# Optimization experiments

Hardware: AMD Instinct MI355X
Metric: run time of the kernel (lower is better)

Reference implementation:

```python
import jax, jax.numpy as jnp
import numpy as np

N = 100000          # active voxels
KS = 7              # kernel size per spatial dim
K = KS ** 3         # 343 kernel offsets
G = 64              # voxel grid extent
INPLANES = 128
PLANES = 128
D2 = PLANES // 4    # 32
EPS = 1e-5


def _build_neighbor_map(seed=0):
    # Random distinct voxel coordinates in a G^3 grid, then for every point and
    # every 7^3 offset find the index of the neighboring voxel (-1 if absent).
    rng = np.random.default_rng(seed)
    lin = rng.choice(G ** 3, size=N, replace=False)
    coords = np.stack(np.unravel_index(lin, (G, G, G)), axis=1).astype(np.int64)  # [N,3]
    keys = coords[:, 0] * G * G + coords[:, 1] * G + coords[:, 2]
    order = np.argsort(keys)
    skeys = keys[order]
    offs = np.arange(KS) - KS // 2
    off_grid = np.stack(np.meshgrid(offs, offs, offs, indexing='ij'), axis=-1).reshape(K, 3)
    q = coords[:, None, :] + off_grid[None, :, :]          # [N,K,3]
    inb = np.all((q >= 0) & (q < G), axis=-1)
    qk = q[..., 0] * G * G + q[..., 1] * G + q[..., 2]
    pos = np.searchsorted(skeys, qk)
    pos_c = np.clip(pos, 0, N - 1)
    found = inb & (skeys[pos_c] == qk)
    nbr = np.where(found, order[pos_c], -1).astype(np.int32)  # [N,K]
    return jnp.asarray(nbr)


def setup_inputs() -> dict:
    key = jax.random.key(0)
    k = jax.random.split(key, 4)
    feats = jax.random.normal(k[0], (N, INPLANES), jnp.float32)
    w1 = jax.random.normal(k[1], (INPLANES, D2), jnp.float32) / np.sqrt(INPLANES)
    w_conv = jax.random.normal(k[2], (K, D2, D2), jnp.float32) / np.sqrt(K * D2)
    w2 = jax.random.normal(k[3], (D2, PLANES), jnp.float32) / np.sqrt(D2)
    return {
        'feats': feats,
        'nbr': _build_neighbor_map(),
        'w1': w1,
        'ln1_g': jnp.ones((D2,), jnp.float32),
        'ln1_b': jnp.zeros((D2,), jnp.float32),
        'w_conv': w_conv,
        'w2': w2,
        'ln2_g': jnp.ones((PLANES,), jnp.float32),
        'ln2_b': jnp.zeros((PLANES,), jnp.float32),
    }


def _layernorm(x, g, b):
    m = jnp.mean(x, axis=-1, keepdims=True)
    v = jnp.var(x, axis=-1, keepdims=True)
    return (x - m) * jax.lax.rsqrt(v + EPS) * g + b


def _sparse_conv(x, nbr, w):
    # x: [N,d2], nbr: [N,K], w: [K,d2,d2]; gather-apply-scatter per kernel offset.
    def step(acc, inp):
        idx, wk = inp                                # idx: [N], wk: [d2,d2]
        valid = (idx >= 0).astype(x.dtype)[:, None]
        g = jnp.take(x, jnp.maximum(idx, 0), axis=0) * valid
        return acc + g @ wk, None
    acc0 = jnp.zeros((x.shape[0], w.shape[2]), x.dtype)
    out, _ = jax.lax.scan(step, acc0, (nbr.T, w))
    return out


def reference(feats, nbr, w1, ln1_g, ln1_b, w_conv, w2, ln2_g, ln2_b):
    shortcut = feats                                  # inplanes == planes -> Identity
    h = _layernorm(feats @ w1, ln1_g, ln1_b)          # unary_1: [N,d2]
    h = _sparse_conv(h, nbr, w_conv)                  # 7^3 sparse conv: [N,d2]
    h = _layernorm(h @ w2, ln2_g, ln2_b)              # unary_2: [N,planes]
    h = jax.nn.gelu(h, approximate=False)             # drop_path is Identity (rate 0)
    return h + shortcut
```

## Files before the change

kernel.cpp:

```cpp
#include <hip/hip_runtime.h>
#include <hip/hip_bf16.h>

#define N_PTS 100000
#define KOFF 343
#define EPS 1e-5f
#define NTILES 3125

typedef __hip_bfloat16 bf16;
typedef __attribute__((ext_vector_type(4))) float f32x4;
typedef __attribute__((ext_vector_type(16))) float f32x16;
typedef __attribute__((ext_vector_type(8))) short s16x8;

__global__ __launch_bounds__(256) void pack_kernel(const float* __restrict__ w_conv,
                                                   bf16* __restrict__ wpk) {
  int t = blockIdx.x * 256 + threadIdx.x;
  if (t >= KOFF * 128) return;
  int l = t & 63;
  int s = (t >> 6) & 1;
  int k = t >> 7;
  int col = l & 31;
  int kq = l >> 5;
  const float* wk = w_conv + k * 1024;
  s16x8 v;
  for (int j = 0; j < 8; ++j) {
    bf16 h = __float2bfloat16(wk[(s * 16 + kq * 8 + j) * 32 + col]);
    short sv;
    __builtin_memcpy(&sv, &h, 2);
    v[j] = sv;
  }
  *reinterpret_cast<s16x8*>(reinterpret_cast<char*>(wpk) + (size_t)t * 16) = v;
}

__global__ __launch_bounds__(256) void unary1_kernel(const float* __restrict__ feats,
    const float* __restrict__ w1, const float* __restrict__ g1,
    const float* __restrict__ b1, bf16* __restrict__ h1b) {
  __shared__ float sf[8][128];
  __shared__ float sw[128 * 32];
  int tid = threadIdx.x;
  int rbase = blockIdx.x * 8;
  if (blockIdx.x == 0 && tid < 16)
    reinterpret_cast<int*>(h1b)[N_PTS * 16 + tid] = 0;
  for (int i = tid; i < 1024; i += 256)
    reinterpret_cast<f32x4*>(sw)[i] = reinterpret_cast<const f32x4*>(w1)[i];
  {
    int i = tid;
    int r = rbase + (i >> 5);
    f32x4 v = reinterpret_cast<const f32x4*>(feats)[(size_t)r * 32 + (i & 31)];
    reinterpret_cast<f32x4*>(&sf[0][0])[i] = v;
  }
  __syncthreads();
  int half = tid >> 5;
  int c = tid & 31;
  int r = rbase + half;
  const float* frow = sf[half];
  float acc = 0.f;
  #pragma unroll 8
  for (int kk = 0; kk < 128; ++kk)
    acc += frow[kk] * sw[kk * 32 + c];
  float s = acc, s2 = acc * acc;
  #pragma unroll
  for (int m = 16; m >= 1; m >>= 1) {
    s  += __shfl_xor(s,  m, 64);
    s2 += __shfl_xor(s2, m, 64);
  }
  float mean = s * (1.f / 32.f);
  float var  = s2 * (1.f / 32.f) - mean * mean;
  float y = (acc - mean) * rsqrtf(var + EPS) * g1[c] + b1[c];
  h1b[(size_t)r * 32 + c] = __float2bfloat16(y);
}

#define SSTRIDE 87

template<int KCNT, int KBASE>
__device__ __forceinline__ void stage_round(const int* __restrict__ g,
                                            int* __restrict__ snbr, int tid) {
  for (int i = tid; i < 32 * KCNT; i += 256) {
    int row = i / KCNT;
    int kk = i - row * KCNT;
    int v = g[row * KOFF + KBASE + kk];
    snbr[row * SSTRIDE + kk] = v < 0 ? N_PTS : v;
  }
}

template<int KCNT, int KBASE>
__device__ __forceinline__ void process_round(const int* __restrict__ snbr,
    const bf16* __restrict__ h1b, const s16x8* __restrict__ wb,
    f32x16& acc, int wave, int l, int col, int kq) {
  int k0 = (KCNT * wave) >> 2;
  int k1 = (KCNT * (wave + 1)) >> 2;
  const int* myrow = snbr + col * SSTRIDE;
  int id0 = myrow[k0];
  int id1 = (k0 + 1 < k1) ? myrow[k0 + 1] : N_PTS;
  for (int kb = k0; kb < k1; kb += 2) {
    int idn0 = (kb + 2 < k1) ? myrow[kb + 2] : N_PTS;
    int idn1 = (kb + 3 < k1) ? myrow[kb + 3] : N_PTS;
    const s16x8* r0 = reinterpret_cast<const s16x8*>(h1b + (size_t)id0 * 32);
    const s16x8* r1 = reinterpret_cast<const s16x8*>(h1b + (size_t)id1 * 32);
    s16x8 A00 = r0[kq], A01 = r0[2 + kq];
    s16x8 A10 = r1[kq], A11 = r1[2 + kq];
    int kg0 = KBASE + kb;
    int kg1 = KBASE + ((kb + 1 < k1) ? kb + 1 : kb);
    s16x8 B00 = wb[(size_t)kg0 * 128 + l];
    s16x8 B01 = wb[(size_t)kg0 * 128 + 64 + l];
    s16x8 B10 = wb[(size_t)kg1 * 128 + l];
    s16x8 B11 = wb[(size_t)kg1 * 128 + 64 + l];
    acc = __builtin_amdgcn_mfma_f32_32x32x16_bf16(A00, B00, acc, 0, 0, 0);
    acc = __builtin_amdgcn_mfma_f32_32x32x16_bf16(A01, B01, acc, 0, 0, 0);
    acc = __builtin_amdgcn_mfma_f32_32x32x16_bf16(A10, B10, acc, 0, 0, 0);
    acc = __builtin_amdgcn_mfma_f32_32x32x16_bf16(A11, B11, acc, 0, 0, 0);
    id0 = idn0; id1 = idn1;
  }
}

__global__ __launch_bounds__(256, 8) void conv_s_kernel(const bf16* __restrict__ h1b,
    const int* __restrict__ nbr, const bf16* __restrict__ wpk,
    float* __restrict__ h2) {
  __shared__ int snbr[4096];
  int tid = threadIdx.x;
  int wave = tid >> 6;
  int l = tid & 63;
  int col = l & 31;
  int kq = l >> 5;
  int pbase = blockIdx.x * 32;
  const int* g = nbr + (size_t)pbase * KOFF;
  const s16x8* wb = reinterpret_cast<const s16x8*>(wpk);
  f32x16 acc;
  #pragma unroll
  for (int i = 0; i < 16; ++i) acc[i] = 0.f;

  stage_round<86, 0>(g, snbr, tid);
  __syncthreads();
  process_round<86, 0>(snbr, h1b, wb, acc, wave, l, col, kq);
  __syncthreads();
  stage_round<86, 86>(g, snbr, tid);
  __syncthreads();
  process_round<86, 86>(snbr, h1b, wb, acc, wave, l, col, kq);
  __syncthreads();
  stage_round<86, 172>(g, snbr, tid);
  __syncthreads();
  process_round<86, 172>(snbr, h1b, wb, acc, wave, l, col, kq);
  __syncthreads();
  stage_round<85, 258>(g, snbr, tid);
  __syncthreads();
  process_round<85, 258>(snbr, h1b, wb, acc, wave, l, col, kq);
  __syncthreads();

  float* red = reinterpret_cast<float*>(snbr);
  #pragma unroll
  for (int reg = 0; reg < 16; ++reg) {
    int rrow = (reg & 3) + 8 * (reg >> 2) + 4 * kq;
    red[wave * 1024 + rrow * 32 + col] = acc[reg];
  }
  __syncthreads();
  const f32x4* rv = reinterpret_cast<const f32x4*>(red);
  f32x4 s = rv[tid] + rv[256 + tid] + rv[512 + tid] + rv[768 + tid];
  reinterpret_cast<f32x4*>(h2 + (size_t)pbase * 32)[tid] = s;
}

__global__ __launch_bounds__(256) void unary2_kernel(const float* __restrict__ h2,
    const float* __restrict__ w2, const float* __restrict__ g2,
    const float* __restrict__ b2, const float* __restrict__ feats,
    float* __restrict__ out) {
  int tid = threadIdx.x;
  int wave = tid >> 6;
  int l = tid & 63;
  int r = blockIdx.x * 4 + wave;
  const float* hrow = h2 + (size_t)r * 32;
  float acc0 = 0.f, acc1 = 0.f;
  #pragma unroll
  for (int q = 0; q < 8; ++q) {
    f32x4 hv = reinterpret_cast<const f32x4*>(hrow)[q];
    #pragma unroll
    for (int j = 0; j < 4; ++j) {
      int kk = q * 4 + j;
      float h = hv[j];
      acc0 += h * w2[kk * 128 + l];
      acc1 += h * w2[kk * 128 + 64 + l];
    }
  }
  float s = acc0 + acc1, s2 = acc0 * acc0 + acc1 * acc1;
  #pragma unroll
  for (int m = 32; m >= 1; m >>= 1) {
    s  += __shfl_xor(s,  m, 64);
    s2 += __shfl_xor(s2, m, 64);
  }
  float mean = s * (1.f / 128.f);
  float var  = s2 * (1.f / 128.f) - mean * mean;
  float inv = rsqrtf(var + EPS);
  float y0 = (acc0 - mean) * inv * g2[l] + b2[l];
  float y1 = (acc1 - mean) * inv * g2[64 + l] + b2[64 + l];
  float ge0 = 0.5f * y0 * (1.f + erff(y0 * 0.70710678118f));
  float ge1 = 0.5f * y1 * (1.f + erff(y1 * 0.70710678118f));
  out[(size_t)r * 128 + l]      = ge0 + feats[(size_t)r * 128 + l];
  out[(size_t)r * 128 + 64 + l] = ge1 + feats[(size_t)r * 128 + 64 + l];
}

extern "C" void kernel_launch(void* const* d_in, const int* in_sizes, int n_in,
                              void* d_out, int out_size, void* d_ws, size_t ws_size,
                              hipStream_t stream) {
  const float* feats  = (const float*)d_in[0];
  const int*   nbr    = (const int*)d_in[1];
  const float* w1     = (const float*)d_in[2];
  const float* ln1_g  = (const float*)d_in[3];
  const float* ln1_b  = (const float*)d_in[4];
  const float* w_conv = (const float*)d_in[5];
  const float* w2     = (const float*)d_in[6];
  const float* ln2_g  = (const float*)d_in[7];
  const float* ln2_b  = (const float*)d_in[8];
  float* out = (float*)d_out;
  char* ws = (char*)d_ws;
  bf16*  h1b = (bf16*)ws;
  bf16*  wpk = (bf16*)(ws + 6400064);
  float* h2  = (float*)(ws + 7102528);

  hipLaunchKernelGGL(pack_kernel,   dim3((KOFF * 128 + 255) / 256), dim3(256), 0, stream, w_conv, wpk);
  hipLaunchKernelGGL(unary1_kernel, dim3(N_PTS / 8),                dim3(256), 0, stream, feats, w1, ln1_g, ln1_b, h1b);
  hipLaunchKernelGGL(conv_s_kernel, dim3(NTILES),                   dim3(256), 0, stream, h1b, nbr, wpk, h2);
  hipLaunchKernelGGL(unary2_kernel, dim3(N_PTS / 4),                dim3(256), 0, stream, h2, w2, ln2_g, ln2_b, feats, out);
}
```

Measured before the change: 370.0 us.

## Process 64 points per conv block, sharing weight fragments across two accumulators

The sparse-conv kernel now handles 64 points per block instead of 32. Each wave keeps two MFMA accumulators, one per 32-point half, and both use the same loaded weight fragments, so weight loads per point are halved. Neighbor indices are staged into LDS in two larger rounds instead of four, which cuts the number of block barriers. The costs are a larger LDS footprint (about 44KB), more registers, a lower occupancy target (launch bound 4) and a bounds guard for the partial last tile.

```diff
diff --git a/kernel.cpp b/kernel.cpp
--- a/kernel.cpp
+++ b/kernel.cpp
@@ -5,6 +5,7 @@
 #define KOFF 343
 #define EPS 1e-5f
 #define NTILES 3125
+#define RSTRIDE 173
 
 typedef __hip_bfloat16 bf16;
 typedef __attribute__((ext_vector_type(4))) float f32x4;
@@ -69,92 +70,99 @@
   h1b[(size_t)r * 32 + c] = __float2bfloat16(y);
 }
 
-#define SSTRIDE 87
-
 template<int KCNT, int KBASE>
-__device__ __forceinline__ void stage_round(const int* __restrict__ g,
-                                            int* __restrict__ snbr, int tid) {
-  for (int i = tid; i < 32 * KCNT; i += 256) {
+__device__ __forceinline__ void stage_round(const int* __restrict__ nbr,
+    int* __restrict__ sbuf, int tid, int pbase) {
+  for (int i = tid; i < 64 * KCNT; i += 256) {
     int row = i / KCNT;
     int kk = i - row * KCNT;
-    int v = g[row * KOFF + KBASE + kk];
-    snbr[row * SSTRIDE + kk] = v < 0 ? N_PTS : v;
+    int p = pbase + row;
+    int v = (p < N_PTS) ? nbr[(size_t)p * KOFF + KBASE + kk] : -1;
+    sbuf[row * RSTRIDE + kk] = v < 0 ? N_PTS : v;
   }
 }
 
 template<int KCNT, int KBASE>
-__device__ __forceinline__ void process_round(const int* __restrict__ snbr,
+__device__ __forceinline__ void process_round(const int* __restrict__ sbuf,
     const bf16* __restrict__ h1b, const s16x8* __restrict__ wb,
-    f32x16& acc, int wave, int l, int col, int kq) {
+    f32x16& acc0, f32x16& acc1, int wave, int l, int col, int kq) {
   int k0 = (KCNT * wave) >> 2;
   int k1 = (KCNT * (wave + 1)) >> 2;
-  const int* myrow = snbr + col * SSTRIDE;
-  int id0 = myrow[k0];
-  int id1 = (k0 + 1 < k1) ? myrow[k0 + 1] : N_PTS;
+  const int* row0 = sbuf + col * RSTRIDE;
+  const int* row1 = sbuf + (32 + col) * RSTRIDE;
+  int i00 = row0[k0];
+  int i10 = row1[k0];
+  int i01 = (k0 + 1 < k1) ? row0[k0 + 1] : N_PTS;
+  int i11 = (k0 + 1 < k1) ? row1[k0 + 1] : N_PTS;
   for (int kb = k0; kb < k1; kb += 2) {
-    int idn0 = (kb + 2 < k1) ? myrow[kb + 2] : N_PTS;
-    int idn1 = (kb + 3 < k1) ? myrow[kb + 3] : N_PTS;
-    const s16x8* r0 = reinterpret_cast<const s16x8*>(h1b + (size_t)id0 * 32);
-    const s16x8* r1 = reinterpret_cast<const s16x8*>(h1b + (size_t)id1 * 32);
-    s16x8 A00 = r0[kq], A01 = r0[2 + kq];
-    s16x8 A10 = r1[kq], A11 = r1[2 + kq];
+    int n00 = (kb + 2 < k1) ? row0[kb + 2] : N_PTS;
+    int n10 = (kb + 2 < k1) ? row1[kb + 2] : N_PTS;
+    int n01 = (kb + 3 < k1) ? row0[kb + 3] : N_PTS;
+    int n11 = (kb + 3 < k1) ? row1[kb + 3] : N_PTS;
+    const s16x8* rA = reinterpret_cast<const s16x8*>(h1b + (size_t)i00 * 32);
+    const s16x8* rB = reinterpret_cast<const s16x8*>(h1b + (size_t)i01 * 32);
+    const s16x8* rC = reinterpret_cast<const s16x8*>(h1b + (size_t)i10 * 32);
+    const s16x8* rD = reinterpret_cast<const s16x8*>(h1b + (size_t)i11 * 32);
+    s16x8 a000 = rA[kq], a001 = rA[2 + kq];
+    s16x8 a010 = rB[kq], a011 = rB[2 + kq];
+    s16x8 a100 = rC[kq], a101 = rC[2 + kq];
+    s16x8 a110 = rD[kq], a111 = rD[2 + kq];
     int kg0 = KBASE + kb;
     int kg1 = KBASE + ((kb + 1 < k1) ? kb + 1 : kb);
-    s16x8 B00 = wb[(size_t)kg0 * 128 + l];
-    s16x8 B01 = wb[(size_t)kg0 * 128 + 64 + l];
-    s16x8 B10 = wb[(size_t)kg1 * 128 + l];
-    s16x8 B11 = wb[(size_t)kg1 * 128 + 64 + l];
-    acc = __builtin_amdgcn_mfma_f32_32x32x16_bf16(A00, B00, acc, 0, 0, 0);
-    acc = __builtin_amdgcn_mfma_f32_32x32x16_bf16(A01, B01, acc, 0, 0, 0);
-    acc = __builtin_amdgcn_mfma_f32_32x32x16_bf16(A10, B10, acc, 0, 0, 0);
-    acc = __builtin_amdgcn_mfma_f32_32x32x16_bf16(A11, B11, acc, 0, 0, 0);
-    id0 = idn0; id1 = idn1;
-  }
-}
-
-__global__ __launch_bounds__(256, 8) void conv_s_kernel(const bf16* __restrict__ h1b,
+    s16x8 b00 = wb[(size_t)kg0 * 128 + l];
+    s16x8 b01 = wb[(size_t)kg0 * 128 + 64 + l];
+    s16x8 b10 = wb[(size_t)kg1 * 128 + l];
+    s16x8 b11 = wb[(size_t)kg1 * 128 + 64 + l];
+    acc0 = __builtin_amdgcn_mfma_f32_32x32x16_bf16(a000, b00, acc0, 0, 0, 0);
+    acc0 = __builtin_amdgcn_mfma_f32_32x32x16_bf16(a001, b01, acc0, 0, 0, 0);
+    acc1 = __builtin_amdgcn_mfma_f32_32x32x16_bf16(a100, b00, acc1, 0, 0, 0);
+    acc1 = __builtin_amdgcn_mfma_f32_32x32x16_bf16(a101, b01, acc1, 0, 0, 0);
+    acc0 = __builtin_amdgcn_mfma_f32_32x32x16_bf16(a010, b10, acc0, 0, 0, 0);
+    acc0 = __builtin_amdgcn_mfma_f32_32x32x16_bf16(a011, b11, acc0, 0, 0, 0);
+    acc1 = __builtin_amdgcn_mfma_f32_32x32x16_bf16(a110, b10, acc1, 0, 0, 0);
+    acc1 = __builtin_amdgcn_mfma_f32_32x32x16_bf16(a111, b11, acc1, 0, 0, 0);
+    i00 = n00; i01 = n01; i10 = n10; i11 = n11;
+  }
+}
+
+__global__ __launch_bounds__(256, 4) void conv2_kernel(const bf16* __restrict__ h1b,
     const int* __restrict__ nbr, const bf16* __restrict__ wpk,
     float* __restrict__ h2) {
-  __shared__ int snbr[4096];
+  __shared__ int sbuf[64 * RSTRIDE];
   int tid = threadIdx.x;
   int wave = tid >> 6;
   int l = tid & 63;
   int col = l & 31;
   int kq = l >> 5;
-  int pbase = blockIdx.x * 32;
-  const int* g = nbr + (size_t)pbase * KOFF;
+  int pbase = blockIdx.x * 64;
   const s16x8* wb = reinterpret_cast<const s16x8*>(wpk);
-  f32x16 acc;
-  #pragma unroll
-  for (int i = 0; i < 16; ++i) acc[i] = 0.f;
-
-  stage_round<86, 0>(g, snbr, tid);
-  __syncthreads();
-  process_round<86, 0>(snbr, h1b, wb, acc, wave, l, col, kq);
-  __syncthreads();
-  stage_round<86, 86>(g, snbr, tid);
-  __syncthreads();
-  process_round<86, 86>(snbr, h1b, wb, acc, wave, l, col, kq);
-  __syncthreads();
-  stage_round<86, 172>(g, snbr, tid);
-  __syncthreads();
-  process_round<86, 172>(snbr, h1b, wb, acc, wave, l, col, kq);
-  __syncthreads();
-  stage_round<85, 258>(g, snbr, tid);
-  __syncthreads();
-  process_round<85, 258>(snbr, h1b, wb, acc, wave, l, col, kq);
-  __syncthreads();
-
-  float* red = reinterpret_cast<float*>(snbr);
+  f32x16 acc0, acc1;
+  #pragma unroll
+  for (int i = 0; i < 16; ++i) { acc0[i] = 0.f; acc1[i] = 0.f; }
+
+  stage_round<172, 0>(nbr, sbuf, tid, pbase);
+  __syncthreads();
+  process_round<172, 0>(sbuf, h1b, wb, acc0, acc1, wave, l, col, kq);
+  __syncthreads();
+  stage_round<171, 172>(nbr, sbuf, tid, pbase);
+  __syncthreads();
+  process_round<171, 172>(sbuf, h1b, wb, acc0, acc1, wave, l, col, kq);
+  __syncthreads();
+
+  float* red = reinterpret_cast<float*>(sbuf);
   #pragma unroll
   for (int reg = 0; reg < 16; ++reg) {
     int rrow = (reg & 3) + 8 * (reg >> 2) + 4 * kq;
-    red[wave * 1024 + rrow * 32 + col] = acc[reg];
+    red[(wave * 2 + 0) * 1024 + rrow * 32 + col] = acc0[reg];
+    red[(wave * 2 + 1) * 1024 + rrow * 32 + col] = acc1[reg];
   }
   __syncthreads();
   const f32x4* rv = reinterpret_cast<const f32x4*>(red);
-  f32x4 s = rv[tid] + rv[256 + tid] + rv[512 + tid] + rv[768 + tid];
-  reinterpret_cast<f32x4*>(h2 + (size_t)pbase * 32)[tid] = s;
+  f32x4 s0 = rv[tid] + rv[512 + tid] + rv[1024 + tid] + rv[1536 + tid];
+  f32x4 s1 = rv[256 + tid] + rv[768 + tid] + rv[1280 + tid] + rv[1792 + tid];
+  f32x4* o = reinterpret_cast<f32x4*>(h2 + (size_t)pbase * 32);
+  o[tid] = s0;
+  if (pbase + 64 <= N_PTS) o[256 + tid] = s1;
 }
 
 __global__ __launch_bounds__(256) void unary2_kernel(const float* __restrict__ h2,
@@ -215,6 +223,6 @@
 
   hipLaunchKernelGGL(pack_kernel,   dim3((KOFF * 128 + 255) / 256), dim3(256), 0, stream, w_conv, wpk);
   hipLaunchKernelGGL(unary1_kernel, dim3(N_PTS / 8),                dim3(256), 0, stream, feats, w1, ln1_g, ln1_b, h1b);
-  hipLaunchKernelGGL(conv_s_kernel, dim3(NTILES),                   dim3(256), 0, stream, h1b, nbr, wpk, h2);
+  hipLaunchKernelGGL(conv2_kernel,  dim3((NTILES + 1) / 2),         dim3(256), 0, stream, h1b, nbr, wpk, h2);
   hipLaunchKernelGGL(unary2_kernel, dim3(N_PTS / 4),                dim3(256), 0, stream, h2, w2, ln2_g, ln2_b, feats, out);
 }
```

Measured after the change: 409.8 us. +10.7%, slower.
